# Kernel optimization log

Hardware: AMD Instinct MI355X
Metric: run time of the kernel (lower is better)

The kernel has to match this reference:

```python
import jax, jax.numpy as jnp
import numpy as np

N = 25000      # nodes
E = 400000     # edges (avg degree 16)
MUL = 32       # multiplicity of each irrep block
NSC = 8        # num_edge_scalar_attr
HID = 64       # radial_neurons
WNUM = 4 * MUL # tp.weight_numel (4 uvu paths x mul 32)
NUM_NEIGH = 16.0
INV_SQRT3 = 1.0 / np.sqrt(3.0)   # component-normalized CG for 1o x 1o -> 0e


def setup_inputs() -> dict:
    key = jax.random.key(0)
    ks = jax.random.split(key, 13)
    return {
        'node_input': jax.random.normal(ks[0], (N, 4 * MUL), jnp.float32),
        'node_attr_input': jax.random.normal(ks[1], (N, 1), jnp.float32),
        'node_attr_output': jax.random.normal(ks[2], (N, 1), jnp.float32),
        'edge_src': jax.random.randint(ks[3], (E,), 0, N),
        'edge_dst': jax.random.randint(ks[4], (E,), 0, N),
        'edge_attr': jax.random.normal(ks[5], (E, 4), jnp.float32),
        'edge_scalar_attr': jax.random.normal(ks[6], (E, NSC), jnp.float32),
        # lin1: FCTP(32x0e+32x1o, 1x0e, 32x0e+32x1o) -> two uvw weight blocks (mul2=1 squeezed)
        'w1_s': jax.random.normal(ks[7], (MUL, MUL), jnp.float32),
        'w1_v': jax.random.normal(ks[8], (MUL, MUL), jnp.float32),
        # radial FC net [8, 64, 128]
        'Wfc1': jax.random.normal(ks[9], (NSC, HID), jnp.float32),
        'Wfc2': jax.random.normal(ks[10], (HID, WNUM), jnp.float32),
        # lin2: FCTP(irreps_mid, 1x0e, 32x0e+32x1o): 2 scalar blocks -> 0e, 2 vector blocks -> 1o
        'w2_s': jax.random.normal(ks[11], (2, MUL, MUL), jnp.float32),
        'w2_v': jax.random.normal(ks[12], (2, MUL, MUL), jnp.float32),
    }


def reference(node_input, node_attr_input, node_attr_output, edge_src, edge_dst,
              edge_attr, edge_scalar_attr, w1_s, w1_v, Wfc1, Wfc2, w2_s, w2_v):
    n = node_input.shape[0]
    # split node features into 32x0e scalars and 32x1o vectors
    xs = node_input[:, :MUL]                      # [N, 32]
    xv = node_input[:, MUL:].reshape(n, MUL, 3)   # [N, 32, 3]
    a = node_attr_input[:, 0]                     # [N]

    # ---- lin1: FullyConnectedTensorProduct with 1x0e attr (per-path alpha = 1/sqrt(mul1*mul2))
    inv1 = 1.0 / np.sqrt(MUL * 1.0)
    xs1 = jnp.einsum('nu,n,uw->nw', xs, a, w1_s) * inv1
    xv1 = jnp.einsum('nui,n,uw->nwi', xv, a, w1_v) * inv1

    # ---- radial FC net (silu MLP, fan-in normalized)
    h = jax.nn.silu(edge_scalar_attr @ Wfc1 * (1.0 / np.sqrt(NSC)))
    w = (h @ Wfc2 * (1.0 / np.sqrt(HID))).reshape(-1, 4, MUL)  # [E, 4 paths, 32]

    # ---- gather source node features per edge
    es = xs1[edge_src]            # [E, 32]
    ev = xv1[edge_src]            # [E, 32, 3]
    ys = edge_attr[:, 0]          # [E]    (0e sh)
    yv = edge_attr[:, 1:4]        # [E, 3] (1o sh)

    # ---- CG tensor product, 4 uvu instructions with per-edge weights
    m0 = w[:, 0] * es * ys[:, None]                                   # 0e x 0e -> 0e
    m3 = w[:, 3] * jnp.einsum('eui,ei->eu', ev, yv) * INV_SQRT3       # 1o x 1o -> 0e
    m1 = w[:, 1][:, :, None] * es[:, :, None] * yv[:, None, :]        # 0e x 1o -> 1o
    m2 = w[:, 2][:, :, None] * ev * ys[:, None, None]                 # 1o x 0e -> 1o
    ne = m0.shape[0]
    edge_features = jnp.concatenate(
        [m0, m3, m1.reshape(ne, 3 * MUL), m2.reshape(ne, 3 * MUL)], axis=1)  # [E, 256]

    # ---- scatter-sum to destination nodes, divide by sqrt(num_neighbors)
    mid = jax.ops.segment_sum(edge_features, edge_dst, num_segments=n)
    mid = mid / np.sqrt(NUM_NEIGH)

    # ---- lin2: FCTP(irreps_mid, 1x0e, 32x0e+32x1o), element norm: alpha = 1/sqrt(2*mul)
    b = node_attr_output[:, 0]
    inv2 = 1.0 / np.sqrt(2.0 * MUL)
    s0 = mid[:, :MUL]
    s1 = mid[:, MUL:2 * MUL]
    v1 = mid[:, 2 * MUL:2 * MUL + 3 * MUL].reshape(n, MUL, 3)
    v2 = mid[:, 2 * MUL + 3 * MUL:].reshape(n, MUL, 3)
    out_s = (jnp.einsum('nu,n,uw->nw', s0, b, w2_s[0]) +
             jnp.einsum('nu,n,uw->nw', s1, b, w2_s[1])) * inv2
    out_v = (jnp.einsum('nui,n,uw->nwi', v1, b, w2_v[0]) +
             jnp.einsum('nui,n,uw->nwi', v2, b, w2_v[1])) * inv2
    return jnp.concatenate([out_s, out_v.reshape(n, 3 * MUL)], axis=1)  # [N, 128]
```

## Files before the change

kernel.cpp:

```cpp
#include <hip/hip_runtime.h>


typedef __attribute__((ext_vector_type(8))) short bf16x8;
typedef __attribute__((ext_vector_type(4))) float f32x4;

__device__ __forceinline__ unsigned bf16r(float x) {
    unsigned u = __float_as_uint(x);
    return (u + 0x7fffu + ((u >> 16) & 1u)) >> 16;
}
__device__ __forceinline__ float bflo(unsigned p) { return __uint_as_float(p << 16); }
__device__ __forceinline__ float bfhi(unsigned p) { return __uint_as_float(p & 0xffff0000u); }

__global__ __launch_bounds__(256) void pre_kernel(
    const float* __restrict__ node_input, const float* __restrict__ attr_in,
    const float* __restrict__ w1s, const float* __restrict__ w1v,
    float* __restrict__ xsv1, int n_nodes,
    const float* __restrict__ Wfc1, const float* __restrict__ Wfc2,
    float* __restrict__ W1s, float* __restrict__ W2T, unsigned short* __restrict__ W2Tb,
    const int* __restrict__ edst, int* __restrict__ counts, int n_edges_count)
{
    int t = blockIdx.x * 256 + threadIdx.x;
    const float inv_sqrt_nsc = 0.35355339059327373f;
    if (t < 8 * 64) W1s[t] = Wfc1[t] * inv_sqrt_nsc;
    if (t < 64 * 128) {
        int r = t >> 7, c = t & 127;
        float v = Wfc2[t] * 0.125f;
        W2T[c * 64 + r] = v;
        W2Tb[c * 64 + r] = (unsigned short)bf16r(v);
    }
    for (int e = t; e < n_edges_count; e += gridDim.x * 256)
        atomicAdd(&counts[edst[e]], 1);

    __shared__ float sWs[1024], sWv[1024], srow[8][128];
    for (int k = threadIdx.x; k < 1024; k += 256) { sWs[k] = w1s[k]; sWv[k] = w1v[k]; }
    int tid = threadIdx.x;
    int j = tid & 127;
    int half = tid >> 7;
    int w = 0, i = 0;
    if (j >= 32) { int jj = j - 32; w = jj / 3; i = jj - 3 * w; }
    const float inv1 = 0.17677669529663687f;
    for (int base = blockIdx.x * 8; base < n_nodes; base += gridDim.x * 8) {
        __syncthreads();
        for (int idx = tid; idx < 1024; idx += 256) {
            int r = idx >> 7, c = idx & 127;
            int n = base + r;
            if (n < n_nodes) srow[r][c] = node_input[(size_t)n * 128 + c];
        }
        __syncthreads();
        #pragma unroll
        for (int rr = 0; rr < 4; rr++) {
            int r = 2 * rr + half;
            int n = base + r;
            if (n < n_nodes) {
                float acc = 0.0f;
                if (j < 32) {
                    #pragma unroll
                    for (int u = 0; u < 32; u++) acc += srow[r][u] * sWs[u * 32 + j];
                } else {
                    #pragma unroll
                    for (int u = 0; u < 32; u++) acc += srow[r][32 + 3 * u + i] * sWv[u * 32 + w];
                }
                xsv1[(size_t)n * 128 + j] = acc * (attr_in[n] * inv1);
            }
        }
    }
}

__global__ __launch_bounds__(1024) void scan_kernel(
    const int* __restrict__ counts, int* __restrict__ offs, int* __restrict__ cursor, int n)
{
    __shared__ int part[1024];
    int tid = threadIdx.x;
    int chunk = (n + 1023) / 1024;
    int begin = tid * chunk;
    int end = begin + chunk; if (end > n) end = n;
    int s = 0;
    for (int i = begin; i < end; i++) s += counts[i];
    part[tid] = s;
    __syncthreads();
    for (int off = 1; off < 1024; off <<= 1) {
        int v = (tid >= off) ? part[tid - off] : 0;
        __syncthreads();
        part[tid] += v;
        __syncthreads();
    }
    int base = (tid == 0) ? 0 : part[tid - 1];
    for (int i = begin; i < end; i++) {
        offs[i] = base; cursor[i] = base;
        base += counts[i];
    }
    if (tid == 1023) offs[n] = part[1023];
}

__global__ __launch_bounds__(256) void scatter_kernel(
    const int* __restrict__ edst, const int* __restrict__ esrc,
    const float* __restrict__ eattr, const float* __restrict__ escal,
    int* __restrict__ cursor,
    int* __restrict__ esrc_s, float4* __restrict__ eattr_s, float4* __restrict__ escal_s,
    int n_edges)
{
    int e = blockIdx.x * 256 + threadIdx.x;
    if (e < n_edges) {
        int d = edst[e];
        int p = atomicAdd(&cursor[d], 1);
        esrc_s[p] = esrc[e];
        eattr_s[p] = *reinterpret_cast<const float4*>(eattr + (size_t)e * 4);
        escal_s[2 * (size_t)p]     = *reinterpret_cast<const float4*>(escal + (size_t)e * 8);
        escal_s[2 * (size_t)p + 1] = *reinterpret_cast<const float4*>(escal + (size_t)e * 8 + 4);
    }
}

#define TPW 8
__global__ __launch_bounds__(256) void edge_mlp_v4(
    const float4* __restrict__ escal_s,
    const float* __restrict__ W1s, const unsigned short* __restrict__ W2Tb,
    unsigned short* __restrict__ wbuf, int n_edges, int nrt)
{
    int tid = threadIdx.x;
    int wv = tid >> 6, l = tid & 63;
    int lm = l & 15, lk = l >> 4;
    int k0 = lk * 8;
    int rt0 = (blockIdx.x * 4 + wv) * TPW;

    bf16x8 bf[8][2];
    #pragma unroll
    for (int t = 0; t < 8; t++) {
        int n = t * 16 + lm;
        bf[t][0] = *reinterpret_cast<const bf16x8*>(W2Tb + n * 64 + k0);
        bf[t][1] = *reinterpret_cast<const bf16x8*>(W2Tb + n * 64 + k0 + 32);
    }

    #pragma unroll 2
    for (int t8 = 0; t8 < TPW; t8++) {
        int rt = rt0 + t8;
        if (rt >= nrt) break;
        int kidx = rt * 16 + lm;

        float q[8];
        if (kidx < n_edges) {
            float4 qa = escal_s[2 * (size_t)kidx];
            float4 qb = escal_s[2 * (size_t)kidx + 1];
            q[0] = qa.x; q[1] = qa.y; q[2] = qa.z; q[3] = qa.w;
            q[4] = qb.x; q[5] = qb.y; q[6] = qb.z; q[7] = qb.w;
        } else {
            #pragma unroll
            for (int i = 0; i < 8; i++) q[i] = 0.f;
        }

        union Af { bf16x8 v; unsigned u[4]; };
        Af af0, af1;
        #pragma unroll
        for (int half = 0; half < 2; half++) {
            int kb = k0 + half * 32;
            float h[8];
            #pragma unroll
            for (int i = 0; i < 8; i++) h[i] = 0.f;
            #pragma unroll
            for (int in = 0; in < 8; in++) {
                float qi = q[in];
                float4 wa = *reinterpret_cast<const float4*>(W1s + in * 64 + kb);
                float4 wb = *reinterpret_cast<const float4*>(W1s + in * 64 + kb + 4);
                h[0] += qi * wa.x; h[1] += qi * wa.y; h[2] += qi * wa.z; h[3] += qi * wa.w;
                h[4] += qi * wb.x; h[5] += qi * wb.y; h[6] += qi * wb.z; h[7] += qi * wb.w;
            }
            unsigned* dst = half ? af1.u : af0.u;
            #pragma unroll
            for (int p = 0; p < 4; p++) {
                float s0 = h[2 * p], s1 = h[2 * p + 1];
                s0 = s0 / (1.0f + __expf(-s0));
                s1 = s1 / (1.0f + __expf(-s1));
                dst[p] = bf16r(s0) | (bf16r(s1) << 16);
            }
        }

        #pragma unroll
        for (int t = 0; t < 8; t++) {
            f32x4 a4 = {0.f, 0.f, 0.f, 0.f};
            a4 = __builtin_amdgcn_mfma_f32_16x16x32_bf16(af0.v, bf[t][0], a4, 0, 0, 0);
            a4 = __builtin_amdgcn_mfma_f32_16x16x32_bf16(af1.v, bf[t][1], a4, 0, 0, 0);
            unsigned s0 = bf16r(a4[0]) | (bf16r(a4[1]) << 16);
            unsigned s1 = bf16r(a4[2]) | (bf16r(a4[3]) << 16);
            *reinterpret_cast<uint2*>(wbuf + ((size_t)(rt * 8 + t) * 256) + l * 4) = make_uint2(s0, s1);
        }
    }
}

__global__ __launch_bounds__(256) void gather_out_kernel(
    const unsigned short* __restrict__ wbuf, const float* __restrict__ xsv1,
    const int* __restrict__ esrc_s, const float4* __restrict__ eattr_s,
    const int* __restrict__ offs, const float* __restrict__ attr_out,
    const float* __restrict__ w2s, const float* __restrict__ w2v,
    float* __restrict__ out, int n_nodes)
{
    __shared__ float sW[4096];
    __shared__ float smid[4][256];

    int tid = threadIdx.x;
    for (int idx = tid; idx < 2048; idx += 256) { sW[idx] = w2s[idx]; sW[2048 + idx] = w2v[idx]; }

    int wv = __builtin_amdgcn_readfirstlane(tid >> 6);
    int L = tid & 63;
    int n = blockIdx.x * 4 + wv;
    int g = L >> 4;

    int be, fbase; bool six;
    if (g == 0)      { be = 2 * L;       fbase = 2 * L;      six = false; }
    else if (g == 1) { be = 2 * L - 32;  fbase = 6 * L - 32; six = true;  }
    else if (g == 2) { be = 6 * L - 160; fbase = 6 * L - 32; six = true;  }
    else             { be = 6 * L - 256; fbase = 2 * L - 64; six = false; }

    const int colpart = ((2 * L) >> 4) * 256 + (((2 * L) & 15) << 2);
    const float inv_sqrt3 = 0.5773502691896258f;
    float a0 = 0.f, a1 = 0.f, a2 = 0.f, a3 = 0.f, a4 = 0.f, a5 = 0.f;

    if (n < n_nodes) {
        int start = offs[n], end = offs[n + 1];

        #define GCOMP(EA, WQ, SEL, X0, X1, X2)                                            \
        {                                                                                 \
            unsigned ulo = ((SEL) & 2) ? (WQ).y : (WQ).x;                                 \
            unsigned uhi = ((SEL) & 2) ? (WQ).w : (WQ).z;                                 \
            float wlo = ((SEL) & 1) ? bfhi(ulo) : bflo(ulo);                              \
            float whi = ((SEL) & 1) ? bfhi(uhi) : bflo(uhi);                              \
            if (g == 0) {                                                                 \
                a0 += wlo * (X0).x * (EA).x;                                              \
                a1 += whi * (X0).y * (EA).x;                                              \
            } else if (g == 1) {                                                          \
                float b0 = wlo * (X0).x, b1 = whi * (X0).y;                               \
                a0 += b0 * (EA).y; a1 += b0 * (EA).z; a2 += b0 * (EA).w;                  \
                a3 += b1 * (EA).y; a4 += b1 * (EA).z; a5 += b1 * (EA).w;                  \
            } else if (g == 2) {                                                          \
                float b0 = wlo * (EA).x, b1 = whi * (EA).x;                               \
                a0 += b0 * (X0).x; a1 += b0 * (X0).y; a2 += b0 * (X1).x;                  \
                a3 += b1 * (X1).y; a4 += b1 * (X2).x; a5 += b1 * (X2).y;                  \
            } else {                                                                      \
                a0 += wlo * ((X0).x * (EA).y + (X0).y * (EA).z + (X1).x * (EA).w) * inv_sqrt3; \
                a1 += whi * ((X1).y * (EA).y + (X2).x * (EA).z + (X2).y * (EA).w) * inv_sqrt3; \
            }                                                                             \
        }

        if (start < end) {
            float4 eaA; uint4 wqA; int selA; float2 xA0, xA1, xA2;
            {
                int srcA = esrc_s[start];
                eaA = eattr_s[start];
                selA = start & 3;
                int epart_ = (start >> 4) * 2048 + (((start >> 2) & 3) << 6);
                wqA = *reinterpret_cast<const uint4*>(wbuf + (size_t)epart_ + colpart);
                const float* __restrict__ nbA = xsv1 + (size_t)srcA * 128;
                xA0 = *reinterpret_cast<const float2*>(nbA + be);
                xA1 = *reinterpret_cast<const float2*>(nbA + be + 2);
                xA2 = *reinterpret_cast<const float2*>(nbA + be + 4);
            }
            int srcB = esrc_s[start + 1];
            for (int k = start + 1; k < end; k++) {
                float4 eaB = eattr_s[k];
                int selB = k & 3;
                int epart_ = (k >> 4) * 2048 + (((k >> 2) & 3) << 6);
                uint4 wqB = *reinterpret_cast<const uint4*>(wbuf + (size_t)epart_ + colpart);
                const float* __restrict__ nbB = xsv1 + (size_t)srcB * 128;
                float2 xB0 = *reinterpret_cast<const float2*>(nbB + be);
                float2 xB1 = *reinterpret_cast<const float2*>(nbB + be + 2);
                float2 xB2 = *reinterpret_cast<const float2*>(nbB + be + 4);
                int srcC = esrc_s[k + 1];
                GCOMP(eaA, wqA, selA, xA0, xA1, xA2);
                eaA = eaB; wqA = wqB; selA = selB;
                xA0 = xB0; xA1 = xB1; xA2 = xB2;
                srcB = srcC;
            }
            GCOMP(eaA, wqA, selA, xA0, xA1, xA2);
        }
        #undef GCOMP
    }

    float* row = &smid[wv][fbase];
    row[0] = a0; row[1] = a1;
    if (six) { row[2] = a2; row[3] = a3; row[4] = a4; row[5] = a5; }
    __syncthreads();

    int h = tid >> 7, j = tid & 127;
    int tw = 0, ti = 0;
    if (j >= 32) { int jj = j - 32; tw = jj / 3; ti = jj - 3 * tw; }
    #pragma unroll
    for (int it = 0; it < 2; it++) {
        int ln = 2 * it + h;
        int nn = blockIdx.x * 4 + ln;
        if (nn < n_nodes) {
            const float* __restrict__ sm = smid[ln];
            float o = 0.0f;
            if (j < 32) {
                #pragma unroll
                for (int u = 0; u < 32; u++)
                    o += sm[u] * sW[u * 32 + j] + sm[32 + u] * sW[1024 + u * 32 + j];
            } else {
                #pragma unroll
                for (int u = 0; u < 32; u++)
                    o += sm[64 + 3 * u + ti] * sW[2048 + u * 32 + tw]
                       + sm[160 + 3 * u + ti] * sW[3072 + u * 32 + tw];
            }
            out[(size_t)nn * 128 + j] = o * (attr_out[nn] * 0.03125f);
        }
    }
}

__global__ __launch_bounds__(256) void edge_kernel_atomic(
    const float* __restrict__ xsv1, const int* __restrict__ esrc, const int* __restrict__ edst,
    const float* __restrict__ eattr, const float* __restrict__ escal,
    const float* __restrict__ W1s, const float* __restrict__ W2T,
    float* __restrict__ mid, int n_edges)
{
    int e = blockIdx.x * 256 + threadIdx.x;
    if (e >= n_edges) return;
    const float4 qa = *reinterpret_cast<const float4*>(escal + (size_t)e * 8);
    const float4 qb = *reinterpret_cast<const float4*>(escal + (size_t)e * 8 + 4);
    float h[64];
    #pragma unroll
    for (int t = 0; t < 64; t++) {
        float acc = qa.x * W1s[t]       + qa.y * W1s[64 + t]
                  + qa.z * W1s[128 + t] + qa.w * W1s[192 + t]
                  + qb.x * W1s[256 + t] + qb.y * W1s[320 + t]
                  + qb.z * W1s[384 + t] + qb.w * W1s[448 + t];
        h[t] = acc / (1.0f + __expf(-acc));
    }
    int src = esrc[e], dst = edst[e];
    const float4 ea = *reinterpret_cast<const float4*>(eattr + (size_t)e * 4);
    const float ys = ea.x, yv0 = ea.y, yv1 = ea.z, yv2 = ea.w;
    const float* __restrict__ nb = xsv1 + (size_t)src * 128;
    float* __restrict__ op = mid + (size_t)dst * 256;
    const float inv_sqrt3 = 0.5773502691896258f;
    for (int u = 0; u < 32; u++) {
        float w0 = 0.f, w1 = 0.f, w2 = 0.f, w3 = 0.f;
        const float* __restrict__ r0 = W2T + (size_t)u * 64;
        const float* __restrict__ r1 = W2T + (size_t)(32 + u) * 64;
        const float* __restrict__ r2 = W2T + (size_t)(64 + u) * 64;
        const float* __restrict__ r3 = W2T + (size_t)(96 + u) * 64;
        #pragma unroll
        for (int t = 0; t < 64; t++) {
            float hv = h[t];
            w0 += hv * r0[t]; w1 += hv * r1[t]; w2 += hv * r2[t]; w3 += hv * r3[t];
        }
        float es  = nb[u];
        float ev0 = nb[32 + 3 * u], ev1 = nb[33 + 3 * u], ev2 = nb[34 + 3 * u];
        atomicAdd(op + u,      w0 * es * ys);
        atomicAdd(op + 32 + u, w3 * (ev0 * yv0 + ev1 * yv1 + ev2 * yv2) * inv_sqrt3);
        float a1 = w1 * es;
        atomicAdd(op + 64 + 3 * u, a1 * yv0);
        atomicAdd(op + 65 + 3 * u, a1 * yv1);
        atomicAdd(op + 66 + 3 * u, a1 * yv2);
        float a2 = w2 * ys;
        atomicAdd(op + 160 + 3 * u, a2 * ev0);
        atomicAdd(op + 161 + 3 * u, a2 * ev1);
        atomicAdd(op + 162 + 3 * u, a2 * ev2);
    }
}

__global__ __launch_bounds__(256) void node_out_kernel(
    const float* __restrict__ mid, const float* __restrict__ attr_out,
    const float* __restrict__ w2s, const float* __restrict__ w2v,
    float* __restrict__ out, int n_nodes)
{
    __shared__ float sS0[1024], sS1[1024], sV0[1024], sV1[1024];
    for (int k = threadIdx.x; k < 1024; k += 256) {
        sS0[k] = w2s[k]; sS1[k] = w2s[1024 + k];
        sV0[k] = w2v[k]; sV1[k] = w2v[1024 + k];
    }
    __syncthreads();
    int j = threadIdx.x & 127;
    int half = threadIdx.x >> 7;
    int w = 0, i = 0;
    if (j >= 32) { int jj = j - 32; w = jj / 3; i = jj - 3 * w; }
    const float scale = 0.125f * 0.25f;
    for (int base = blockIdx.x * 2; base < n_nodes; base += gridDim.x * 2) {
        int n = base + half;
        if (n >= n_nodes) continue;
        const float* __restrict__ mr = mid + (size_t)n * 256;
        float acc = 0.0f;
        if (j < 32) {
            #pragma unroll
            for (int u = 0; u < 32; u++)
                acc += mr[u] * sS0[u * 32 + j] + mr[32 + u] * sS1[u * 32 + j];
        } else {
            #pragma unroll
            for (int u = 0; u < 32; u++)
                acc += mr[64 + 3 * u + i] * sV0[u * 32 + w] + mr[160 + 3 * u + i] * sV1[u * 32 + w];
        }
        out[(size_t)n * 128 + j] = acc * (attr_out[n] * scale);
    }
}

extern "C" void kernel_launch(void* const* d_in, const int* in_sizes, int n_in,
                              void* d_out, int out_size, void* d_ws, size_t ws_size,
                              hipStream_t stream)
{
    const float* node_input = (const float*)d_in[0];
    const float* attr_in    = (const float*)d_in[1];
    const float* attr_out   = (const float*)d_in[2];
    const int*   esrc       = (const int*)d_in[3];
    const int*   edst       = (const int*)d_in[4];
    const float* eattr      = (const float*)d_in[5];
    const float* escal      = (const float*)d_in[6];
    const float* w1s        = (const float*)d_in[7];
    const float* w1v        = (const float*)d_in[8];
    const float* Wfc1       = (const float*)d_in[9];
    const float* Wfc2       = (const float*)d_in[10];
    const float* w2s        = (const float*)d_in[11];
    const float* w2v        = (const float*)d_in[12];
    float* out = (float*)d_out;

    int n_nodes = in_sizes[0] / 128;
    int n_edges = in_sizes[3];
    int nrt = (n_edges + 15) / 16;
    int nwave = (nrt + TPW - 1) / TPW;
    int nblk = (nwave + 3) / 4;

    char* p = (char*)d_ws;
    auto alloc = [&](size_t bytes, size_t align) -> void* {
        size_t a = (size_t)p; a = (a + align - 1) & ~(align - 1);
        p = (char*)a; void* r = (void*)p; p += bytes; return r;
    };
    float* xsv1 = (float*)alloc((size_t)n_nodes * 128 * 4, 16);
    float* W1s  = (float*)alloc(512 * 4, 16);
    float* W2T  = (float*)alloc(8192 * 4, 16);
    float* mid  = (float*)alloc((size_t)n_nodes * 256 * 4, 16);
    int* counts = (int*)alloc((size_t)n_nodes * 4, 16);
    int* offs   = (int*)alloc(((size_t)n_nodes + 1) * 4, 16);
    int* cursor = (int*)alloc((size_t)n_nodes * 4, 16);
    int* esrc_s = (int*)alloc(((size_t)n_edges + 4) * 4, 16);
    float4* eattr_s = (float4*)alloc((size_t)n_edges * 16, 16);
    float4* escal_s = (float4*)alloc((size_t)n_edges * 32, 16);
    unsigned short* W2Tb = (unsigned short*)alloc(8192 * 2, 64);
    unsigned short* wbuf = (unsigned short*)alloc((size_t)nrt * 8 * 256 * 2, 64);
    size_t needed = (size_t)(p - (char*)d_ws);

    if (ws_size >= needed) {
        hipMemsetAsync(counts, 0, (size_t)n_nodes * sizeof(int), stream);
        pre_kernel<<<2048, 256, 0, stream>>>(
            node_input, attr_in, w1s, w1v, xsv1, n_nodes,
            Wfc1, Wfc2, W1s, W2T, W2Tb, edst, counts, n_edges);
        scan_kernel<<<1, 1024, 0, stream>>>(counts, offs, cursor, n_nodes);
        scatter_kernel<<<(n_edges + 255) / 256, 256, 0, stream>>>(
            edst, esrc, eattr, escal, cursor, esrc_s, eattr_s, escal_s, n_edges);
        edge_mlp_v4<<<nblk, 256, 0, stream>>>(escal_s, W1s, W2Tb, wbuf, n_edges, nrt);
        gather_out_kernel<<<(n_nodes + 3) / 4, 256, 0, stream>>>(
            wbuf, xsv1, esrc_s, eattr_s, offs, attr_out, w2s, w2v, out, n_nodes);
    } else {
        pre_kernel<<<2048, 256, 0, stream>>>(
            node_input, attr_in, w1s, w1v, xsv1, n_nodes,
            Wfc1, Wfc2, W1s, W2T, W2Tb, edst, counts, 0 );
        hipMemsetAsync(mid, 0, (size_t)n_nodes * 256 * sizeof(float), stream);
        edge_kernel_atomic<<<(n_edges + 255) / 256, 256, 0, stream>>>(
            xsv1, esrc, edst, eattr, escal, W1s, W2T, mid, n_edges);
        node_out_kernel<<<2048, 256, 0, stream>>>(mid, attr_out, w2s, w2v, out, n_nodes);
    }
}
```

Measured before the change: 248.2 us.

## Fuse radial MLP into per-node gather kernel via LDS weight tile

Removes the separate edge MLP kernel and its global bf16 weight buffer. Each wave now computes the radial MLP (SiLU layer plus MFMA) for its node's incoming edges in chunks of 16, writes the per-edge weights to a shared-memory tile and consumes them in the gather loop. This avoids one launch and a global write/read round trip of the per-edge weights. In exchange, nodes with few edges waste MFMA rows, each block loads the W2 fragments into registers, and LDS use grows, which may reduce occupancy. No barrier separates the LDS writes from the cross-lane reads within the wave, so correctness relies on wave-level ordering.

```diff
diff --git a/kernel.cpp b/kernel.cpp
--- a/kernel.cpp
+++ b/kernel.cpp
@@ -110,167 +110,154 @@
     }
 }
 
-#define TPW 8
-__global__ __launch_bounds__(256) void edge_mlp_v4(
+__global__ __launch_bounds__(256) void gather_all_kernel(
     const float4* __restrict__ escal_s,
-    const float* __restrict__ W1s, const unsigned short* __restrict__ W2Tb,
-    unsigned short* __restrict__ wbuf, int n_edges, int nrt)
-{
+    const float* __restrict__ W1s_g, const unsigned short* __restrict__ W2Tb,
+    const float* __restrict__ xsv1, const int* __restrict__ esrc_s,
+    const float4* __restrict__ eattr_s, const int* __restrict__ offs,
+    const float* __restrict__ attr_out,
+    const float* __restrict__ w2s, const float* __restrict__ w2v,
+    float* __restrict__ out, int n_nodes)
+{
+    __shared__ float sW[4096];
+    __shared__ float smid[4][256];
+    __shared__ unsigned short wtile[4][2048];
+
     int tid = threadIdx.x;
-    int wv = tid >> 6, l = tid & 63;
-    int lm = l & 15, lk = l >> 4;
+    for (int idx = tid; idx < 2048; idx += 256) { sW[idx] = w2s[idx]; sW[2048 + idx] = w2v[idx]; }
+
+    int wv = __builtin_amdgcn_readfirstlane(tid >> 6);
+    int L = tid & 63;
+    int n = blockIdx.x * 4 + wv;
+    int lm = L & 15, lk = L >> 4;
     int k0 = lk * 8;
-    int rt0 = (blockIdx.x * 4 + wv) * TPW;
 
     bf16x8 bf[8][2];
     #pragma unroll
     for (int t = 0; t < 8; t++) {
-        int n = t * 16 + lm;
-        bf[t][0] = *reinterpret_cast<const bf16x8*>(W2Tb + n * 64 + k0);
-        bf[t][1] = *reinterpret_cast<const bf16x8*>(W2Tb + n * 64 + k0 + 32);
-    }
-
-    #pragma unroll 2
-    for (int t8 = 0; t8 < TPW; t8++) {
-        int rt = rt0 + t8;
-        if (rt >= nrt) break;
-        int kidx = rt * 16 + lm;
-
-        float q[8];
-        if (kidx < n_edges) {
-            float4 qa = escal_s[2 * (size_t)kidx];
-            float4 qb = escal_s[2 * (size_t)kidx + 1];
-            q[0] = qa.x; q[1] = qa.y; q[2] = qa.z; q[3] = qa.w;
-            q[4] = qb.x; q[5] = qb.y; q[6] = qb.z; q[7] = qb.w;
-        } else {
-            #pragma unroll
-            for (int i = 0; i < 8; i++) q[i] = 0.f;
-        }
-
-        union Af { bf16x8 v; unsigned u[4]; };
-        Af af0, af1;
-        #pragma unroll
-        for (int half = 0; half < 2; half++) {
-            int kb = k0 + half * 32;
-            float h[8];
-            #pragma unroll
-            for (int i = 0; i < 8; i++) h[i] = 0.f;
-            #pragma unroll
-            for (int in = 0; in < 8; in++) {
-                float qi = q[in];
-                float4 wa = *reinterpret_cast<const float4*>(W1s + in * 64 + kb);
-                float4 wb = *reinterpret_cast<const float4*>(W1s + in * 64 + kb + 4);
-                h[0] += qi * wa.x; h[1] += qi * wa.y; h[2] += qi * wa.z; h[3] += qi * wa.w;
-                h[4] += qi * wb.x; h[5] += qi * wb.y; h[6] += qi * wb.z; h[7] += qi * wb.w;
-            }
-            unsigned* dst = half ? af1.u : af0.u;
-            #pragma unroll
-            for (int p = 0; p < 4; p++) {
-                float s0 = h[2 * p], s1 = h[2 * p + 1];
-                s0 = s0 / (1.0f + __expf(-s0));
-                s1 = s1 / (1.0f + __expf(-s1));
-                dst[p] = bf16r(s0) | (bf16r(s1) << 16);
-            }
-        }
-
-        #pragma unroll
-        for (int t = 0; t < 8; t++) {
-            f32x4 a4 = {0.f, 0.f, 0.f, 0.f};
-            a4 = __builtin_amdgcn_mfma_f32_16x16x32_bf16(af0.v, bf[t][0], a4, 0, 0, 0);
-            a4 = __builtin_amdgcn_mfma_f32_16x16x32_bf16(af1.v, bf[t][1], a4, 0, 0, 0);
-            unsigned s0 = bf16r(a4[0]) | (bf16r(a4[1]) << 16);
-            unsigned s1 = bf16r(a4[2]) | (bf16r(a4[3]) << 16);
-            *reinterpret_cast<uint2*>(wbuf + ((size_t)(rt * 8 + t) * 256) + l * 4) = make_uint2(s0, s1);
-        }
-    }
-}
-
-__global__ __launch_bounds__(256) void gather_out_kernel(
-    const unsigned short* __restrict__ wbuf, const float* __restrict__ xsv1,
-    const int* __restrict__ esrc_s, const float4* __restrict__ eattr_s,
-    const int* __restrict__ offs, const float* __restrict__ attr_out,
-    const float* __restrict__ w2s, const float* __restrict__ w2v,
-    float* __restrict__ out, int n_nodes)
-{
-    __shared__ float sW[4096];
-    __shared__ float smid[4][256];
-
-    int tid = threadIdx.x;
-    for (int idx = tid; idx < 2048; idx += 256) { sW[idx] = w2s[idx]; sW[2048 + idx] = w2v[idx]; }
-
-    int wv = __builtin_amdgcn_readfirstlane(tid >> 6);
-    int L = tid & 63;
-    int n = blockIdx.x * 4 + wv;
+        int nn = t * 16 + lm;
+        bf[t][0] = *reinterpret_cast<const bf16x8*>(W2Tb + nn * 64 + k0);
+        bf[t][1] = *reinterpret_cast<const bf16x8*>(W2Tb + nn * 64 + k0 + 32);
+    }
+
     int g = L >> 4;
-
     int be, fbase; bool six;
     if (g == 0)      { be = 2 * L;       fbase = 2 * L;      six = false; }
     else if (g == 1) { be = 2 * L - 32;  fbase = 6 * L - 32; six = true;  }
     else if (g == 2) { be = 6 * L - 160; fbase = 6 * L - 32; six = true;  }
     else             { be = 6 * L - 256; fbase = 2 * L - 64; six = false; }
-
     const int colpart = ((2 * L) >> 4) * 256 + (((2 * L) & 15) << 2);
     const float inv_sqrt3 = 0.5773502691896258f;
     float a0 = 0.f, a1 = 0.f, a2 = 0.f, a3 = 0.f, a4 = 0.f, a5 = 0.f;
 
     if (n < n_nodes) {
         int start = offs[n], end = offs[n + 1];
-
-        #define GCOMP(EA, WQ, SEL, X0, X1, X2)                                            \
-        {                                                                                 \
-            unsigned ulo = ((SEL) & 2) ? (WQ).y : (WQ).x;                                 \
-            unsigned uhi = ((SEL) & 2) ? (WQ).w : (WQ).z;                                 \
-            float wlo = ((SEL) & 1) ? bfhi(ulo) : bflo(ulo);                              \
-            float whi = ((SEL) & 1) ? bfhi(uhi) : bflo(uhi);                              \
-            if (g == 0) {                                                                 \
-                a0 += wlo * (X0).x * (EA).x;                                              \
-                a1 += whi * (X0).y * (EA).x;                                              \
-            } else if (g == 1) {                                                          \
-                float b0 = wlo * (X0).x, b1 = whi * (X0).y;                               \
-                a0 += b0 * (EA).y; a1 += b0 * (EA).z; a2 += b0 * (EA).w;                  \
-                a3 += b1 * (EA).y; a4 += b1 * (EA).z; a5 += b1 * (EA).w;                  \
-            } else if (g == 2) {                                                          \
-                float b0 = wlo * (EA).x, b1 = whi * (EA).x;                               \
-                a0 += b0 * (X0).x; a1 += b0 * (X0).y; a2 += b0 * (X1).x;                  \
-                a3 += b1 * (X1).y; a4 += b1 * (X2).x; a5 += b1 * (X2).y;                  \
-            } else {                                                                      \
-                a0 += wlo * ((X0).x * (EA).y + (X0).y * (EA).z + (X1).x * (EA).w) * inv_sqrt3; \
-                a1 += whi * ((X1).y * (EA).y + (X2).x * (EA).z + (X2).y * (EA).w) * inv_sqrt3; \
-            }                                                                             \
-        }
-
-        if (start < end) {
-            float4 eaA; uint4 wqA; int selA; float2 xA0, xA1, xA2;
+        unsigned short* __restrict__ wt = wtile[wv];
+
+        for (int cbase = start; cbase < end; cbase += 16) {
+            int cnt = end - cbase; if (cnt > 16) cnt = 16;
+
+            float q[8];
+            if (lm < cnt) {
+                float4 qa = escal_s[2 * (size_t)(cbase + lm)];
+                float4 qb = escal_s[2 * (size_t)(cbase + lm) + 1];
+                q[0] = qa.x; q[1] = qa.y; q[2] = qa.z; q[3] = qa.w;
+                q[4] = qb.x; q[5] = qb.y; q[6] = qb.z; q[7] = qb.w;
+            } else {
+                #pragma unroll
+                for (int z = 0; z < 8; z++) q[z] = 0.f;
+            }
+            union Af { bf16x8 v; unsigned u[4]; };
+            Af af0, af1;
+            #pragma unroll
+            for (int half = 0; half < 2; half++) {
+                int kb = k0 + half * 32;
+                float h[8];
+                #pragma unroll
+                for (int z = 0; z < 8; z++) h[z] = 0.f;
+                #pragma unroll
+                for (int in = 0; in < 8; in++) {
+                    float qi = q[in];
+                    float4 wa = *reinterpret_cast<const float4*>(W1s_g + in * 64 + kb);
+                    float4 wb = *reinterpret_cast<const float4*>(W1s_g + in * 64 + kb + 4);
+                    h[0] += qi * wa.x; h[1] += qi * wa.y; h[2] += qi * wa.z; h[3] += qi * wa.w;
+                    h[4] += qi * wb.x; h[5] += qi * wb.y; h[6] += qi * wb.z; h[7] += qi * wb.w;
+                }
+                unsigned* dst = half ? af1.u : af0.u;
+                #pragma unroll
+                for (int p = 0; p < 4; p++) {
+                    float s0 = h[2 * p], s1 = h[2 * p + 1];
+                    s0 = s0 / (1.0f + __expf(-s0));
+                    s1 = s1 / (1.0f + __expf(-s1));
+                    dst[p] = bf16r(s0) | (bf16r(s1) << 16);
+                }
+            }
+
+            #pragma unroll
+            for (int t = 0; t < 8; t++) {
+                f32x4 a4 = {0.f, 0.f, 0.f, 0.f};
+                a4 = __builtin_amdgcn_mfma_f32_16x16x32_bf16(af0.v, bf[t][0], a4, 0, 0, 0);
+                a4 = __builtin_amdgcn_mfma_f32_16x16x32_bf16(af1.v, bf[t][1], a4, 0, 0, 0);
+                unsigned s0 = bf16r(a4[0]) | (bf16r(a4[1]) << 16);
+                unsigned s1 = bf16r(a4[2]) | (bf16r(a4[3]) << 16);
+                *reinterpret_cast<uint2*>(&wt[t * 256 + L * 4]) = make_uint2(s0, s1);
+            }
+
+            #define GCOMP(EA, WQ, SEL, X0, X1, X2)                                            \
+            {                                                                                 \
+                unsigned ulo = ((SEL) & 2) ? (WQ).y : (WQ).x;                                 \
+                unsigned uhi = ((SEL) & 2) ? (WQ).w : (WQ).z;                                 \
+                float wlo = ((SEL) & 1) ? bfhi(ulo) : bflo(ulo);                              \
+                float whi = ((SEL) & 1) ? bfhi(uhi) : bflo(uhi);                              \
+                if (g == 0) {                                                                 \
+                    a0 += wlo * (X0).x * (EA).x;                                              \
+                    a1 += whi * (X0).y * (EA).x;                                              \
+                } else if (g == 1) {                                                          \
+                    float b0 = wlo * (X0).x, b1 = whi * (X0).y;                               \
+                    a0 += b0 * (EA).y; a1 += b0 * (EA).z; a2 += b0 * (EA).w;                  \
+                    a3 += b1 * (EA).y; a4 += b1 * (EA).z; a5 += b1 * (EA).w;                  \
+                } else if (g == 2) {                                                          \
+                    float b0 = wlo * (EA).x, b1 = whi * (EA).x;                               \
+                    a0 += b0 * (X0).x; a1 += b0 * (X0).y; a2 += b0 * (X1).x;                  \
+                    a3 += b1 * (X1).y; a4 += b1 * (X2).x; a5 += b1 * (X2).y;                  \
+                } else {                                                                      \
+                    a0 += wlo * ((X0).x * (EA).y + (X0).y * (EA).z + (X1).x * (EA).w) * inv_sqrt3; \
+                    a1 += whi * ((X1).y * (EA).y + (X2).x * (EA).z + (X2).y * (EA).w) * inv_sqrt3; \
+                }                                                                             \
+            }
+
             {
-                int srcA = esrc_s[start];
-                eaA = eattr_s[start];
-                selA = start & 3;
-                int epart_ = (start >> 4) * 2048 + (((start >> 2) & 3) << 6);
-                wqA = *reinterpret_cast<const uint4*>(wbuf + (size_t)epart_ + colpart);
-                const float* __restrict__ nbA = xsv1 + (size_t)srcA * 128;
-                xA0 = *reinterpret_cast<const float2*>(nbA + be);
-                xA1 = *reinterpret_cast<const float2*>(nbA + be + 2);
-                xA2 = *reinterpret_cast<const float2*>(nbA + be + 4);
-            }
-            int srcB = esrc_s[start + 1];
-            for (int k = start + 1; k < end; k++) {
-                float4 eaB = eattr_s[k];
-                int selB = k & 3;
-                int epart_ = (k >> 4) * 2048 + (((k >> 2) & 3) << 6);
-                uint4 wqB = *reinterpret_cast<const uint4*>(wbuf + (size_t)epart_ + colpart);
-                const float* __restrict__ nbB = xsv1 + (size_t)srcB * 128;
-                float2 xB0 = *reinterpret_cast<const float2*>(nbB + be);
-                float2 xB1 = *reinterpret_cast<const float2*>(nbB + be + 2);
-                float2 xB2 = *reinterpret_cast<const float2*>(nbB + be + 4);
-                int srcC = esrc_s[k + 1];
+                float4 eaA; uint4 wqA; int selA; float2 xA0, xA1, xA2;
+                {
+                    int srcA = esrc_s[cbase];
+                    eaA = eattr_s[cbase];
+                    selA = 0;
+                    wqA = *reinterpret_cast<const uint4*>(&wt[colpart]);
+                    const float* __restrict__ nbA = xsv1 + (size_t)srcA * 128;
+                    xA0 = *reinterpret_cast<const float2*>(nbA + be);
+                    xA1 = *reinterpret_cast<const float2*>(nbA + be + 2);
+                    xA2 = *reinterpret_cast<const float2*>(nbA + be + 4);
+                }
+                int srcB = esrc_s[cbase + 1];
+                for (int m = 1; m < cnt; m++) {
+                    int k = cbase + m;
+                    float4 eaB = eattr_s[k];
+                    int selB = m & 3;
+                    uint4 wqB = *reinterpret_cast<const uint4*>(&wt[colpart + ((m >> 2) << 6)]);
+                    const float* __restrict__ nbB = xsv1 + (size_t)srcB * 128;
+                    float2 xB0 = *reinterpret_cast<const float2*>(nbB + be);
+                    float2 xB1 = *reinterpret_cast<const float2*>(nbB + be + 2);
+                    float2 xB2 = *reinterpret_cast<const float2*>(nbB + be + 4);
+                    int srcC = esrc_s[k + 1];
+                    GCOMP(eaA, wqA, selA, xA0, xA1, xA2);
+                    eaA = eaB; wqA = wqB; selA = selB;
+                    xA0 = xB0; xA1 = xB1; xA2 = xB2;
+                    srcB = srcC;
+                }
                 GCOMP(eaA, wqA, selA, xA0, xA1, xA2);
-                eaA = eaB; wqA = wqB; selA = selB;
-                xA0 = xB0; xA1 = xB1; xA2 = xB2;
-                srcB = srcC;
-            }
-            GCOMP(eaA, wqA, selA, xA0, xA1, xA2);
-        }
-        #undef GCOMP
+            }
+            #undef GCOMP
+        }
     }
 
     float* row = &smid[wv][fbase];
@@ -409,9 +396,6 @@
 
     int n_nodes = in_sizes[0] / 128;
     int n_edges = in_sizes[3];
-    int nrt = (n_edges + 15) / 16;
-    int nwave = (nrt + TPW - 1) / TPW;
-    int nblk = (nwave + 3) / 4;
 
     char* p = (char*)d_ws;
     auto alloc = [&](size_t bytes, size_t align) -> void* {
@@ -429,7 +413,6 @@
     float4* eattr_s = (float4*)alloc((size_t)n_edges * 16, 16);
     float4* escal_s = (float4*)alloc((size_t)n_edges * 32, 16);
     unsigned short* W2Tb = (unsigned short*)alloc(8192 * 2, 64);
-    unsigned short* wbuf = (unsigned short*)alloc((size_t)nrt * 8 * 256 * 2, 64);
     size_t needed = (size_t)(p - (char*)d_ws);
 
     if (ws_size >= needed) {
@@ -440,9 +423,9 @@
         scan_kernel<<<1, 1024, 0, stream>>>(counts, offs, cursor, n_nodes);
         scatter_kernel<<<(n_edges + 255) / 256, 256, 0, stream>>>(
             edst, esrc, eattr, escal, cursor, esrc_s, eattr_s, escal_s, n_edges);
-        edge_mlp_v4<<<nblk, 256, 0, stream>>>(escal_s, W1s, W2Tb, wbuf, n_edges, nrt);
-        gather_out_kernel<<<(n_nodes + 3) / 4, 256, 0, stream>>>(
-            wbuf, xsv1, esrc_s, eattr_s, offs, attr_out, w2s, w2v, out, n_nodes);
+        gather_all_kernel<<<(n_nodes + 3) / 4, 256, 0, stream>>>(
+            escal_s, W1s, W2Tb, xsv1, esrc_s, eattr_s, offs,
+            attr_out, w2s, w2v, out, n_nodes);
     } else {
         pre_kernel<<<2048, 256, 0, stream>>>(
             node_input, attr_in, w1s, w1v, xsv1, n_nodes,
```

Result: slower. 353.0 us (+42.2%).
